# Performance work log

Hardware: AMD Instinct MI355X
Metric: run time of the kernel (lower is better)

## Reference

```python
import jax, jax.numpy as jnp
import numpy as np

N_QUBITS = 12
N_LAYERS = 4
BATCH = 1024


def _apply_1q(state, G, w, n):
    # state: (b, 2**n) complex; G: (2,2) shared or (b,2,2) batched gate on wire w
    b = state.shape[0]
    st = state.reshape(b, 2**w, 2, 2**(n - w - 1))
    if G.ndim == 3:
        out = jnp.einsum('bij,bljr->blir', G, st)
    else:
        out = jnp.einsum('ij,bljr->blir', G, st)
    return out.reshape(b, -1)


def _apply_cnot(state, c, t, n):
    # CNOT with control c, target t; reshape so both wire axes are explicit
    b = state.shape[0]
    q0, q1 = (c, t) if c < t else (t, c)
    st = state.reshape(b, 2**q0, 2, 2**(q1 - q0 - 1), 2, 2**(n - q1 - 1))
    if c < t:
        # control axis = 2; flip target axis in the control=1 slice
        out = jnp.stack([st[:, :, 0], jnp.flip(st[:, :, 1], axis=3)], axis=2)
    else:
        # control axis = 4; target axis sits at position 2 of the slice
        out = jnp.stack([st[:, :, :, :, 0], jnp.flip(st[:, :, :, :, 1], axis=2)], axis=4)
    return out.reshape(b, -1)


def _vqc_forward(x, weights):
    b, n = x.shape
    L = weights.shape[0]
    state = jnp.zeros((b, 2**n), jnp.complex64).at[:, 0].set(1.0)
    # AngleEmbedding (default rotation='X'): RX(x[:, w]) on wire w, batched gates
    half = x.astype(jnp.float32) * 0.5
    c, s = jnp.cos(half), jnp.sin(half)
    for w in range(n):
        G = jnp.stack([jnp.stack([c[:, w] + 0j, -1j * s[:, w]], -1),
                       jnp.stack([-1j * s[:, w], c[:, w] + 0j], -1)], -2)  # (b,2,2)
        state = _apply_1q(state, G, w, n)
    # StronglyEntanglingLayers: per layer, Rot(phi,theta,omega) on each wire,
    # then ring of CNOTs with range r = l % (n-1) + 1
    for l in range(L):
        for w in range(n):
            phi, theta, omega = weights[l, w, 0], weights[l, w, 1], weights[l, w, 2]
            ct, sn = jnp.cos(theta * 0.5), jnp.sin(theta * 0.5)
            ep = jnp.exp(0.5j * (phi + omega))
            em = jnp.exp(-0.5j * (phi + omega))
            ed = jnp.exp(0.5j * (phi - omega))
            edc = jnp.exp(-0.5j * (phi - omega))
            # Rot = RZ(omega) @ RY(theta) @ RZ(phi)
            G = jnp.stack([jnp.stack([em * ct, -ed * sn]),
                           jnp.stack([edc * sn, ep * ct])])  # (2,2)
            state = _apply_1q(state, G, w, n)
        r = l % (n - 1) + 1
        for w in range(n):
            state = _apply_cnot(state, w, (w + r) % n, n)
    # <Z_w> = sum over basis states of probs * (+1 if bit w == 0 else -1)
    probs = state.real**2 + state.imag**2
    evs = []
    for w in range(n):
        p = probs.reshape(b, 2**w, 2, -1)
        evs.append(p[:, :, 0, :].sum(axis=(1, 2)) - p[:, :, 1, :].sum(axis=(1, 2)))
    return jnp.stack(evs, axis=1)  # (b, n_qubits)


def setup_inputs() -> dict:
    key = jax.random.key(0)
    k1, k2 = jax.random.split(key)
    x = jax.random.uniform(k1, (BATCH, N_QUBITS), jnp.float32) * np.float32(np.pi)
    weights = jax.random.normal(k2, (N_LAYERS, N_QUBITS, 3), jnp.float32)
    return {"x": x, "weights": weights}


def reference(x, weights):
    return _vqc_forward(x, weights)
```

## Files before the change

kernel.cpp:

```cpp
#include <hip/hip_runtime.h>

#define NQ 12
#define NL 4
typedef __attribute__((ext_vector_type(2))) float f32x2;


__device__ __forceinline__ f32x2 cmul(f32x2 a, f32x2 b) {
    f32x2 r; r.x = a.x*b.x - a.y*b.y; r.y = a.x*b.y + a.y*b.x; return r;
}

__device__ __forceinline__ int SW(int i) {
    return i ^ ((((i >> 4) ^ (i >> 8)) & 7) << 1);
}

template<int P>
__device__ __forceinline__ void ry16(f32x2 (&v)[16], float ct, float sn) {
#pragma unroll
    for (int r0 = 0; r0 < 16; ++r0) {
        if (!(r0 & (1 << P))) {
            const int r1 = r0 | (1 << P);
            const f32x2 a0 = v[r0], a1 = v[r1];
            v[r0] = ct*a0 - sn*a1;
            v[r1] = sn*a0 + ct*a1;
        }
    }
}

__device__ __forceinline__ void ry4grp(f32x2 (&v)[16], const f32x2* rc) {
    const f32x2 c0 = rc[0], c1 = rc[1], c2 = rc[2], c3 = rc[3];
    ry16<3>(v, c0.x, c0.y);
    ry16<2>(v, c1.x, c1.y);
    ry16<1>(v, c2.x, c2.y);
    ry16<0>(v, c3.x, c3.y);
}

__device__ __forceinline__ void diag_rz(f32x2 (&v)[16], f32x2 tc, const f32x2* fz) {
    const f32x2 f0 = fz[0], f1 = fz[1], f2 = fz[2], f3 = fz[3];
#pragma unroll
    for (int r = 0; r < 16; ++r) v[r] = cmul(v[r], tc);
#pragma unroll
    for (int r = 8; r < 16; ++r) v[r] = cmul(v[r], f0);
#pragma unroll
    for (int r = 0; r < 16; ++r) if (r & 4) v[r] = cmul(v[r], f1);
#pragma unroll
    for (int r = 0; r < 16; ++r) if (r & 2) v[r] = cmul(v[r], f2);
#pragma unroll
    for (int r = 0; r < 16; ++r) if (r & 1) v[r] = cmul(v[r], f3);
}

__device__ constexpr int foldG(int rho, int r) {
    int g = 0;
    if (rho == 1) {
        if (r & 1) g ^= 0xC01; if (r & 2) g ^= 0x003;
        if (r & 4) g ^= 0x006; if (r & 8) g ^= 0x00C;
    } else if (rho == 2) {
        if (r & 1) g ^= 0x501; if (r & 2) g ^= 0xA02;
        if (r & 4) g ^= 0x005; if (r & 8) g ^= 0x00A;
    } else {
        if (r & 1) g ^= 0x241; if (r & 2) g ^= 0x482;
        if (r & 4) g ^= 0x904; if (r & 8) g ^= 0x009;
    }
    return g;
}

template<int RHO>
__device__ __forceinline__ void readCA(f32x2 (&v)[16], const f32x2* buf, int t) {
    int F;
    if constexpr (RHO == 1) F = (t << 4) ^ ((t & 127) << 3) ^ ((t >> 7) << 10);
    else if constexpr (RHO == 2) F = (t << 4) ^ ((t & 255) << 2);
    else F = (t << 4) ^ ((t & 255) << 1);
#pragma unroll
    for (int r = 0; r < 16; ++r)
        v[r] = buf[SW(F ^ foldG(RHO, r))];
}

__device__ __forceinline__ void permA_write(const f32x2 (&v)[16], f32x2* buf, int t) {
    float4* b4 = (float4*)buf;
    const int base = t << 4;
#pragma unroll
    for (int r = 0; r < 16; r += 2) {
        const int a = SW(base | r);
        b4[a >> 1] = make_float4(v[r].x, v[r].y, v[r+1].x, v[r+1].y);
    }
}
__device__ __forceinline__ void permB_read(f32x2 (&v)[16], const f32x2* buf, int t) {
    const int hi = (t & 0xF0) << 4, lo = t & 15;
#pragma unroll
    for (int r = 0; r < 16; ++r) v[r] = buf[SW(hi | (r << 4) | lo)];
}
__device__ __forceinline__ void permB_write(const f32x2 (&v)[16], f32x2* buf, int t) {
    const int hi = (t & 0xF0) << 4, lo = t & 15;
#pragma unroll
    for (int r = 0; r < 16; ++r) buf[SW(hi | (r << 4) | lo)] = v[r];
}
__device__ __forceinline__ void permC_read(f32x2 (&v)[16], const f32x2* buf, int t) {
#pragma unroll
    for (int r = 0; r < 16; ++r) v[r] = buf[SW((r << 8) | t)];
}
__device__ __forceinline__ void permC_write(const f32x2 (&v)[16], f32x2* buf, int t) {
#pragma unroll
    for (int r = 0; r < 16; ++r) buf[SW((r << 8) | t)] = v[r];
}

__device__ __forceinline__ void embed(f32x2 (&v)[16], const float* __restrict__ xr, int t) {
    float cw[NQ], sw[NQ];
#pragma unroll
    for (int w = 0; w < NQ; ++w) __sincosf(0.5f * xr[w], &sw[w], &cw[w]);
    float lm = 1.f;
#pragma unroll
    for (int k = 0; k < 8; ++k) lm *= ((t >> k) & 1) ? sw[7-k] : cw[7-k];
    const int pt = __popc(t) & 3;
    float pre[4], pim[4];
#pragma unroll
    for (int q = 0; q < 4; ++q) {
        const int kk = (pt + q) & 3;
        pre[q] = (kk == 0) ? 1.f : ((kk == 2) ? -1.f : 0.f);
        pim[q] = (kk == 1) ? -1.f : ((kk == 3) ? 1.f : 0.f);
    }
#pragma unroll
    for (int r = 0; r < 16; ++r) {
        float m = lm;
        m *= (r & 1) ? sw[11] : cw[11];
        m *= (r & 2) ? sw[10] : cw[10];
        m *= (r & 4) ? sw[9]  : cw[9];
        m *= (r & 8) ? sw[8]  : cw[8];
        const int pc = __popc(r) & 3;
        v[r].x = m * pre[pc];
        v[r].y = m * pim[pc];
    }
}

__device__ __forceinline__ void meas(const f32x2 (&v)[16], float (&ev)[NQ], int t) {
    float S0 = 0.f, S8 = 0.f, S4 = 0.f, S2 = 0.f, S1 = 0.f;
#pragma unroll
    for (int r = 0; r < 16; ++r) {
        const float p = v[r].x*v[r].x + v[r].y*v[r].y;
        S0 += p;
        S8 += (r & 8) ? -p : p;
        S4 += (r & 4) ? -p : p;
        S2 += (r & 2) ? -p : p;
        S1 += (r & 1) ? -p : p;
    }
    const float g88 = (__popc(t & 0x88) & 1) ? -1.f : 1.f;
    const float g44 = (__popc(t & 0x44) & 1) ? -1.f : 1.f;
    const float g22 = (__popc(t & 0x22) & 1) ? -1.f : 1.f;
    const float g11 = (__popc(t & 0x11) & 1) ? -1.f : 1.f;
    const float g80 = (t & 0x80) ? -1.f : 1.f;
    const float g40 = (t & 0x40) ? -1.f : 1.f;
    const float g20 = (t & 0x20) ? -1.f : 1.f;
    const float g10 = (t & 0x10) ? -1.f : 1.f;
    ev[0] = g88 * S0;  ev[1] = g44 * S0;  ev[2]  = g22 * S0;  ev[3]  = g11 * S0;
    ev[4] = g80 * S8;  ev[5] = g40 * S4;  ev[6]  = g20 * S2;  ev[7]  = g10 * S1;
    ev[8] = g88 * S8;  ev[9] = g44 * S4;  ev[10] = g22 * S2;  ev[11] = g11 * S1;
}

__global__ __launch_bounds__(256) void vqc_kernel(
    const float* __restrict__ x,
    const float* __restrict__ wts,
    float* __restrict__ out)
{
    __shared__ alignas(16) f32x2 buf[4096];
    __shared__ alignas(16) f32x2 rcs[NL * NQ];
    __shared__ alignas(16) f32x2 rzP[NL][4];
    __shared__ alignas(16) f32x2 rzW[3][4];
    __shared__ float offs[8];
    __shared__ float red[2][4][NQ];

    const int t  = threadIdx.x;
    const int b0 = blockIdx.x * 2, b1 = b0 + 1;

    if (t < NL * NQ) {
        float s, c; __sincosf(0.5f * wts[t*3 + 1], &s, &c);
        f32x2 tv = {c, s}; rcs[t] = tv;
    } else if (t < 64) {
        const int u = t - 48, l = u >> 2, j = u & 3;
        float s, c; __sincosf(wts[(l*NQ + 8 + j)*3 + 0], &s, &c);
        f32x2 tv = {c, s}; rzP[l][j] = tv;
    } else if (t < 76) {
        const int u = t - 64, l = u >> 2, j = u & 3;
        float s, c; __sincosf(wts[(l*NQ + j)*3 + 2], &s, &c);
        f32x2 tv = {c, s}; rzW[l][j] = tv;
    } else if (t < 80) {
        const int l = t - 76;
        float s = 0.f;
#pragma unroll
        for (int j = 0; j < 4; ++j) s += wts[(l*NQ + 8 + j)*3 + 0];
        offs[l] = -0.5f * s;
    } else if (t < 83) {
        const int l = t - 80;
        float s = 0.f;
#pragma unroll
        for (int j = 0; j < 4; ++j) s += wts[(l*NQ + j)*3 + 2];
        offs[4 + l] = -0.5f * s;
    }

    f32x2 v0[16], v1[16];
    embed(v0, x + b0*NQ, t);
    embed(v1, x + b1*NQ, t);
    __syncthreads();

#pragma unroll 1
    for (int l = 0; l < NL; ++l) {
        float aP = offs[l];
#pragma unroll
        for (int k = 0; k < 8; ++k)
            aP += (((t >> k) & 1) ? 0.5f : -0.5f) * wts[(l*NQ + (7-k))*3 + 0];
        float sp, cp; __sincosf(aP, &sp, &cp);
        f32x2 tcP = {cp, sp};
        diag_rz(v0, tcP, rzP[l]);
        diag_rz(v1, tcP, rzP[l]);
        ry4grp(v0, &rcs[l*NQ + 8]);
        ry4grp(v1, &rcs[l*NQ + 8]);

        __syncthreads(); permA_write(v0, buf, t);
        __syncthreads(); permB_read(v0, buf, t);
        __syncthreads(); permA_write(v1, buf, t);
        __syncthreads(); permB_read(v1, buf, t);
        ry4grp(v0, &rcs[l*NQ + 4]);
        ry4grp(v1, &rcs[l*NQ + 4]);

        __syncthreads(); permB_write(v0, buf, t);
        __syncthreads(); permC_read(v0, buf, t);
        __syncthreads(); permB_write(v1, buf, t);
        __syncthreads(); permC_read(v1, buf, t);
        ry4grp(v0, &rcs[l*NQ + 0]);
        ry4grp(v1, &rcs[l*NQ + 0]);

        if (l == NL - 1) break;

        float aW = offs[4 + l];
#pragma unroll
        for (int k = 0; k < 8; ++k)
            aW += (((t >> k) & 1) ? 0.5f : -0.5f) * wts[(l*NQ + (11-k))*3 + 2];
        float so, co; __sincosf(aW, &so, &co);
        f32x2 tcW = {co, so};
        diag_rz(v0, tcW, rzW[l]);
        diag_rz(v1, tcW, rzW[l]);

        __syncthreads(); permC_write(v0, buf, t);
        __syncthreads();
        if (l == 0)      readCA<1>(v0, buf, t);
        else if (l == 1) readCA<2>(v0, buf, t);
        else             readCA<3>(v0, buf, t);
        __syncthreads(); permC_write(v1, buf, t);
        __syncthreads();
        if (l == 0)      readCA<1>(v1, buf, t);
        else if (l == 1) readCA<2>(v1, buf, t);
        else             readCA<3>(v1, buf, t);
    }

    float ev0[NQ], ev1[NQ];
    meas(v0, ev0, t);
    meas(v1, ev1, t);
#pragma unroll
    for (int w = 0; w < NQ; ++w) {
#pragma unroll
        for (int off = 32; off; off >>= 1) {
            ev0[w] += __shfl_xor(ev0[w], off, 64);
            ev1[w] += __shfl_xor(ev1[w], off, 64);
        }
    }
    if ((t & 63) == 0) {
#pragma unroll
        for (int w = 0; w < NQ; ++w) {
            red[0][t >> 6][w] = ev0[w];
            red[1][t >> 6][w] = ev1[w];
        }
    }
    __syncthreads();
    if (t < NQ)
        out[b0*NQ + t] = red[0][0][t] + red[0][1][t] + red[0][2][t] + red[0][3][t];
    else if (t >= 64 && t < 64 + NQ) {
        const int w = t - 64;
        out[b1*NQ + w] = red[1][0][w] + red[1][1][w] + red[1][2][w] + red[1][3][w];
    }
}

extern "C" void kernel_launch(void* const* d_in, const int* in_sizes, int n_in,
                              void* d_out, int out_size, void* d_ws, size_t ws_size,
                              hipStream_t stream) {
    const float* x   = (const float*)d_in[0];
    const float* wts = (const float*)d_in[1];
    float* out = (float*)d_out;
    const int nb2 = (in_sizes[0] / NQ) / 2;
    vqc_kernel<<<dim3(nb2), dim3(256), 0, stream>>>(x, wts, out);
}
```

Baseline: 53.49 us.

## Process one batch element per block and drop barriers around wave-local permutation

Each block now handles one batch element instead of two, so the grid doubles from 512 to 1024 blocks. The per-thread register state halves, which may raise occupancy. The A-to-B permutation through shared memory is now guarded only by an lgkmcnt wait instead of block barriers, on the assumption that it stays within a wavefront. The other barriers are cut down too. The cost is less work per block to hide latency and a correctness risk if the permA/permB exchange actually crosses wavefronts.

```diff
diff --git a/kernel.cpp b/kernel.cpp
--- a/kernel.cpp
+++ b/kernel.cpp
@@ -130,30 +130,6 @@
     }
 }
 
-__device__ __forceinline__ void meas(const f32x2 (&v)[16], float (&ev)[NQ], int t) {
-    float S0 = 0.f, S8 = 0.f, S4 = 0.f, S2 = 0.f, S1 = 0.f;
-#pragma unroll
-    for (int r = 0; r < 16; ++r) {
-        const float p = v[r].x*v[r].x + v[r].y*v[r].y;
-        S0 += p;
-        S8 += (r & 8) ? -p : p;
-        S4 += (r & 4) ? -p : p;
-        S2 += (r & 2) ? -p : p;
-        S1 += (r & 1) ? -p : p;
-    }
-    const float g88 = (__popc(t & 0x88) & 1) ? -1.f : 1.f;
-    const float g44 = (__popc(t & 0x44) & 1) ? -1.f : 1.f;
-    const float g22 = (__popc(t & 0x22) & 1) ? -1.f : 1.f;
-    const float g11 = (__popc(t & 0x11) & 1) ? -1.f : 1.f;
-    const float g80 = (t & 0x80) ? -1.f : 1.f;
-    const float g40 = (t & 0x40) ? -1.f : 1.f;
-    const float g20 = (t & 0x20) ? -1.f : 1.f;
-    const float g10 = (t & 0x10) ? -1.f : 1.f;
-    ev[0] = g88 * S0;  ev[1] = g44 * S0;  ev[2]  = g22 * S0;  ev[3]  = g11 * S0;
-    ev[4] = g80 * S8;  ev[5] = g40 * S4;  ev[6]  = g20 * S2;  ev[7]  = g10 * S1;
-    ev[8] = g88 * S8;  ev[9] = g44 * S4;  ev[10] = g22 * S2;  ev[11] = g11 * S1;
-}
-
 __global__ __launch_bounds__(256) void vqc_kernel(
     const float* __restrict__ x,
     const float* __restrict__ wts,
@@ -164,10 +140,10 @@
     __shared__ alignas(16) f32x2 rzP[NL][4];
     __shared__ alignas(16) f32x2 rzW[3][4];
     __shared__ float offs[8];
-    __shared__ float red[2][4][NQ];
-
-    const int t  = threadIdx.x;
-    const int b0 = blockIdx.x * 2, b1 = b0 + 1;
+    __shared__ float red[4][NQ];
+
+    const int t = threadIdx.x;
+    const int b = blockIdx.x;
 
     if (t < NL * NQ) {
         float s, c; __sincosf(0.5f * wts[t*3 + 1], &s, &c);
@@ -194,9 +170,8 @@
         offs[4 + l] = -0.5f * s;
     }
 
-    f32x2 v0[16], v1[16];
-    embed(v0, x + b0*NQ, t);
-    embed(v1, x + b1*NQ, t);
+    f32x2 v[16];
+    embed(v, x + b*NQ, t);
     __syncthreads();
 
 #pragma unroll 1
@@ -207,24 +182,20 @@
             aP += (((t >> k) & 1) ? 0.5f : -0.5f) * wts[(l*NQ + (7-k))*3 + 0];
         float sp, cp; __sincosf(aP, &sp, &cp);
         f32x2 tcP = {cp, sp};
-        diag_rz(v0, tcP, rzP[l]);
-        diag_rz(v1, tcP, rzP[l]);
-        ry4grp(v0, &rcs[l*NQ + 8]);
-        ry4grp(v1, &rcs[l*NQ + 8]);
-
-        __syncthreads(); permA_write(v0, buf, t);
-        __syncthreads(); permB_read(v0, buf, t);
-        __syncthreads(); permA_write(v1, buf, t);
-        __syncthreads(); permB_read(v1, buf, t);
-        ry4grp(v0, &rcs[l*NQ + 4]);
-        ry4grp(v1, &rcs[l*NQ + 4]);
-
-        __syncthreads(); permB_write(v0, buf, t);
-        __syncthreads(); permC_read(v0, buf, t);
-        __syncthreads(); permB_write(v1, buf, t);
-        __syncthreads(); permC_read(v1, buf, t);
-        ry4grp(v0, &rcs[l*NQ + 0]);
-        ry4grp(v1, &rcs[l*NQ + 0]);
+        diag_rz(v, tcP, rzP[l]);
+        ry4grp(v, &rcs[l*NQ + 8]);
+
+        permA_write(v, buf, t);
+        asm volatile("s_waitcnt lgkmcnt(0)" ::: "memory");
+        permB_read(v, buf, t);
+
+        ry4grp(v, &rcs[l*NQ + 4]);
+
+        permB_write(v, buf, t);
+        __syncthreads();
+        permC_read(v, buf, t);
+
+        ry4grp(v, &rcs[l*NQ + 0]);
 
         if (l == NL - 1) break;
 
@@ -234,46 +205,52 @@
             aW += (((t >> k) & 1) ? 0.5f : -0.5f) * wts[(l*NQ + (11-k))*3 + 2];
         float so, co; __sincosf(aW, &so, &co);
         f32x2 tcW = {co, so};
-        diag_rz(v0, tcW, rzW[l]);
-        diag_rz(v1, tcW, rzW[l]);
-
-        __syncthreads(); permC_write(v0, buf, t);
-        __syncthreads();
-        if (l == 0)      readCA<1>(v0, buf, t);
-        else if (l == 1) readCA<2>(v0, buf, t);
-        else             readCA<3>(v0, buf, t);
-        __syncthreads(); permC_write(v1, buf, t);
-        __syncthreads();
-        if (l == 0)      readCA<1>(v1, buf, t);
-        else if (l == 1) readCA<2>(v1, buf, t);
-        else             readCA<3>(v1, buf, t);
-    }
-
-    float ev0[NQ], ev1[NQ];
-    meas(v0, ev0, t);
-    meas(v1, ev1, t);
-#pragma unroll
-    for (int w = 0; w < NQ; ++w) {
-#pragma unroll
-        for (int off = 32; off; off >>= 1) {
-            ev0[w] += __shfl_xor(ev0[w], off, 64);
-            ev1[w] += __shfl_xor(ev1[w], off, 64);
-        }
-    }
+        diag_rz(v, tcW, rzW[l]);
+
+        __syncthreads();
+        permC_write(v, buf, t);
+        __syncthreads();
+        if (l == 0)      readCA<1>(v, buf, t);
+        else if (l == 1) readCA<2>(v, buf, t);
+        else             readCA<3>(v, buf, t);
+        __syncthreads();
+    }
+
+    float S0 = 0.f, S8 = 0.f, S4 = 0.f, S2 = 0.f, S1 = 0.f;
+#pragma unroll
+    for (int r = 0; r < 16; ++r) {
+        const float p = v[r].x*v[r].x + v[r].y*v[r].y;
+        S0 += p;
+        S8 += (r & 8) ? -p : p;
+        S4 += (r & 4) ? -p : p;
+        S2 += (r & 2) ? -p : p;
+        S1 += (r & 1) ? -p : p;
+    }
+    const float g88 = (__popc(t & 0x88) & 1) ? -1.f : 1.f;
+    const float g44 = (__popc(t & 0x44) & 1) ? -1.f : 1.f;
+    const float g22 = (__popc(t & 0x22) & 1) ? -1.f : 1.f;
+    const float g11 = (__popc(t & 0x11) & 1) ? -1.f : 1.f;
+    const float g80 = (t & 0x80) ? -1.f : 1.f;
+    const float g40 = (t & 0x40) ? -1.f : 1.f;
+    const float g20 = (t & 0x20) ? -1.f : 1.f;
+    const float g10 = (t & 0x10) ? -1.f : 1.f;
+
+    float ev[NQ];
+    ev[0] = g88 * S0;  ev[1] = g44 * S0;  ev[2]  = g22 * S0;  ev[3]  = g11 * S0;
+    ev[4] = g80 * S8;  ev[5] = g40 * S4;  ev[6]  = g20 * S2;  ev[7]  = g10 * S1;
+    ev[8] = g88 * S8;  ev[9] = g44 * S4;  ev[10] = g22 * S2;  ev[11] = g11 * S1;
+
+#pragma unroll
+    for (int w = 0; w < NQ; ++w)
+#pragma unroll
+        for (int off = 32; off; off >>= 1)
+            ev[w] += __shfl_xor(ev[w], off, 64);
     if ((t & 63) == 0) {
 #pragma unroll
-        for (int w = 0; w < NQ; ++w) {
-            red[0][t >> 6][w] = ev0[w];
-            red[1][t >> 6][w] = ev1[w];
-        }
+        for (int w = 0; w < NQ; ++w) red[t >> 6][w] = ev[w];
     }
     __syncthreads();
-    if (t < NQ)
-        out[b0*NQ + t] = red[0][0][t] + red[0][1][t] + red[0][2][t] + red[0][3][t];
-    else if (t >= 64 && t < 64 + NQ) {
-        const int w = t - 64;
-        out[b1*NQ + w] = red[1][0][w] + red[1][1][w] + red[1][2][w] + red[1][3][w];
-    }
+    if (t < NQ) out[b*NQ + t] = red[0][t] + red[1][t] + red[2][t] + red[3][t];
 }
 
 extern "C" void kernel_launch(void* const* d_in, const int* in_sizes, int n_in,
@@ -282,6 +259,6 @@
     const float* x   = (const float*)d_in[0];
     const float* wts = (const float*)d_in[1];
     float* out = (float*)d_out;
-    const int nb2 = (in_sizes[0] / NQ) / 2;
-    vqc_kernel<<<dim3(nb2), dim3(256), 0, stream>>>(x, wts, out);
-}
+    const int nb = in_sizes[0] / NQ;
+    vqc_kernel<<<dim3(nb), dim3(256), 0, stream>>>(x, wts, out);
+}
```

After: 44.80 us. -16.2%, faster.
